# Optimization experiments

Hardware: AMD Instinct MI355X
Metric: run time of the kernel (lower is better)

## Reference

```python
import jax, jax.numpy as jnp
import numpy as np

B, S, D, H = 4, 1024, 1024, 16
HD = D // H  # head_dim = 64
MASKED_BIAS = -10000.0


def setup_inputs() -> dict:
    key = jax.random.key(0)
    ks = jax.random.split(key, 7)
    sc = 0.02
    return {
        "hidden_states": jax.random.normal(ks[0], (B, S, D), jnp.float32),
        "textual_key": jax.random.normal(ks[1], (B, H, S, HD), jnp.float32),
        "textual_value": jax.random.normal(ks[2], (B, H, S, HD), jnp.float32),
        "Wc": jax.random.normal(ks[3], (D, 3 * D), jnp.float32) * sc,  # Conv1D c_attn
        "bc": jnp.zeros((3 * D,), jnp.float32),
        "Wp": jax.random.normal(ks[4], (D, D), jnp.float32) * sc,  # Conv1D c_proj
        "bp": jnp.zeros((D,), jnp.float32),
    }


def reference(hidden_states, textual_key, textual_value, Wc, bc, Wp, bp):
    b, s, d = hidden_states.shape
    # Conv1D: x @ W + b, then split into q, k, v
    qkv = hidden_states @ Wc + bc  # [B,S,3D]
    q, k, v = jnp.split(qkv, 3, axis=-1)

    def split_heads(t):  # [B,S,D] -> [B,H,S,HD]
        return t.reshape(b, s, H, HD).transpose(0, 2, 1, 3)

    q, k, v = split_heads(q), split_heads(k), split_heads(v)

    # cross-key scores against textual past + fused elementwise self-term
    text_w = jnp.einsum("bhqd,bhkd->bhqk", q, textual_key)  # [B,H,S,S_kv]
    self_w = jnp.sum(q * k, axis=-1, keepdims=True)  # [B,H,S,1]
    attn_w = jnp.concatenate([text_w, self_w], axis=-1) / (HD ** 0.5)

    # nonResidual causal mask: bias[kl-ql:kl, 1:kl+1] (strict lower-tri since
    # columns are shifted by 1) concatenated with an always-true self column
    i = jnp.arange(s)
    causal = i[None, :] < i[:, None]  # [S,S_kv]: allow k < q (strict)
    mask = jnp.concatenate([causal, jnp.ones((s, 1), bool)], axis=-1)[None, None]
    attn_w = jnp.where(mask, attn_w, jnp.asarray(MASKED_BIAS, attn_w.dtype))
    attn_w = jax.nn.softmax(attn_w, axis=-1)

    w_rest, w_self = attn_w[..., :-1], attn_w[..., -1:]
    out = jnp.einsum("bhqk,bhkd->bhqd", w_rest, textual_value) + w_self * v

    out = out.transpose(0, 2, 1, 3).reshape(b, s, d)  # merge heads
    return out @ Wp + bp
```

## Files before the change

kernel.cpp:

```cpp
#include <hip/hip_runtime.h>

typedef __bf16 bf16_t;
typedef __bf16 bf16x8 __attribute__((ext_vector_type(8)));
typedef __bf16 bf16x4 __attribute__((ext_vector_type(4)));
typedef float f32x4 __attribute__((ext_vector_type(4)));

__device__ __forceinline__ void gl_lds16(const bf16_t* g, bf16_t* l) {
  __builtin_amdgcn_global_load_lds(
      (const __attribute__((address_space(1))) unsigned int*)g,
      (__attribute__((address_space(3))) unsigned int*)l, 16, 0, 0);
}

__global__ __launch_bounds__(256) void prep_kernel(
    const float* __restrict__ hs, const float* __restrict__ tk, const float* __restrict__ tv,
    const float* __restrict__ Wc, const float* __restrict__ Wp,
    bf16_t* __restrict__ Ahs, bf16_t* __restrict__ Ktb, bf16_t* __restrict__ Vtb,
    bf16_t* __restrict__ WcT, bf16_t* __restrict__ WpT) {
  const int blk = blockIdx.x;
  if (blk < 8192) {
    const float4* src = (blk < 4096) ? (const float4*)hs : (const float4*)tk;
    bf16x4* dst = (blk < 4096) ? (bf16x4*)Ahs : (bf16x4*)Ktb;
    int i = (blk & 4095) * 256 + threadIdx.x;
    float4 v = src[i];
    bf16x4 o;
    o[0] = (bf16_t)v.x; o[1] = (bf16_t)v.y; o[2] = (bf16_t)v.z; o[3] = (bf16_t)v.w;
    dst[i] = o;
  } else {
    __shared__ float tile[32][33];
    const int x = threadIdx.x & 31, y0 = threadIdx.x >> 5;
    const float* in; bf16_t* out; int R, C, c0, r0; size_t base;
    if (blk < 11264) {
      int t = blk - 8192; in = Wc; out = WcT; R = 1024; C = 3072; base = 0;
      c0 = (t % 96) * 32; r0 = (t / 96) * 32;
    } else if (blk < 12288) {
      int t = blk - 11264; in = Wp; out = WpT; R = 1024; C = 1024; base = 0;
      c0 = (t & 31) * 32; r0 = (t >> 5) * 32;
    } else {
      int t = blk - 12288; int z = t >> 6, rest = t & 63;
      in = tv; out = Vtb; R = 1024; C = 64; base = (size_t)z * 65536;
      c0 = (rest & 1) * 32; r0 = (rest >> 1) * 32;
    }
#pragma unroll
    for (int k = 0; k < 4; k++) {
      int y = y0 + 8 * k;
      tile[y][x] = in[base + (size_t)(r0 + y) * C + c0 + x];
    }
    __syncthreads();
#pragma unroll
    for (int k = 0; k < 4; k++) {
      int y = y0 + 8 * k;
      out[base + (size_t)(c0 + y) * R + r0 + x] = (bf16_t)tile[x][y];
    }
  }
}

__global__ __launch_bounds__(256) void gemm_qkv_kernel(
    const bf16_t* __restrict__ A, const bf16_t* __restrict__ Bt, const float* __restrict__ bias,
    bf16_t* __restrict__ Qo, bf16_t* __restrict__ Ko, bf16_t* __restrict__ Vo) {
  __shared__ __align__(16) bf16_t smem[16384];
  bf16_t* Asm = smem;
  bf16_t* Bsm = smem + 8192;
  const int tid = threadIdx.x;
  const int wave = tid >> 6, lane = tid & 63;
  const int c = lane & 15, qd = lane >> 4;
  const int wm = (wave & 1) * 64, wn = (wave >> 1) * 64;
  const int m0 = blockIdx.y * 128, n0 = blockIdx.x * 128;

  f32x4 acc[4][4];
#pragma unroll
  for (int i = 0; i < 4; i++)
#pragma unroll
    for (int j = 0; j < 4; j++) acc[i][j] = (f32x4){0.f, 0.f, 0.f, 0.f};

  for (int kt = 0; kt < 1024; kt += 64) {
#pragma unroll
    for (int p = 0; p < 4; p++) {
      int chunk = p * 256 + tid;
      int row = chunk >> 3, sb = chunk & 7;
      int kb = sb ^ (row & 7);
      gl_lds16(A + (size_t)(m0 + row) * 1024 + kt + kb * 8, &Asm[chunk * 8]);
      gl_lds16(Bt + (size_t)(n0 + row) * 1024 + kt + kb * 8, &Bsm[chunk * 8]);
    }
    __syncthreads();
#pragma unroll
    for (int kk = 0; kk < 2; kk++) {
      bf16x8 af[4], bfr[4];
#pragma unroll
      for (int i = 0; i < 4; i++) {
        int row = wm + 16 * i + c;
        af[i] = *(const bf16x8*)(&Asm[row * 64 + (((4 * kk + qd) ^ (row & 7)) << 3)]);
      }
#pragma unroll
      for (int j = 0; j < 4; j++) {
        int row = wn + 16 * j + c;
        bfr[j] = *(const bf16x8*)(&Bsm[row * 64 + (((4 * kk + qd) ^ (row & 7)) << 3)]);
      }
#pragma unroll
      for (int i = 0; i < 4; i++)
#pragma unroll
        for (int j = 0; j < 4; j++)
          acc[i][j] = __builtin_amdgcn_mfma_f32_16x16x32_bf16(af[i], bfr[j], acc[i][j], 0, 0, 0);
    }
    __syncthreads();
  }
#pragma unroll
  for (int j = 0; j < 4; j++) {
    int n = n0 + wn + 16 * j + c;
    float bv = bias[n];
    int col = wn + 16 * j + c;
#pragma unroll
    for (int i = 0; i < 4; i++) {
#pragma unroll
      for (int r = 0; r < 4; r++) {
        int row = wm + 16 * i + 4 * qd + r;
        int chunk = col >> 3;
        smem[row * 128 + (((chunk ^ (row & 15)) << 3)) + (col & 7)] = (bf16_t)(acc[i][j][r] + bv);
      }
    }
  }
  __syncthreads();
  {
    int row = tid >> 1, half = tid & 1;
    int m = m0 + row, bb = m >> 10, s = m & 1023;
    int nb = n0 + half * 64;
    int type = nb >> 10, d = nb & 1023, h = d >> 6;
    bf16_t* dst = ((type == 0) ? Qo : (type == 1) ? Ko : Vo) +
                  (((size_t)bb * 16 + h) * 1024 + s) * 64;
#pragma unroll
    for (int k = 0; k < 8; k++) {
      int chunk = half * 8 + k;
      bf16x8 v = *(const bf16x8*)(&smem[row * 128 + ((chunk ^ (row & 15)) << 3)]);
      *(bf16x8*)(dst + k * 8) = v;
    }
  }
}

__global__ __launch_bounds__(256) void gemm_out_kernel(
    const bf16_t* __restrict__ A, const bf16_t* __restrict__ Bt, const float* __restrict__ bias,
    float* __restrict__ out) {
  __shared__ bf16_t Asm[2][8192];
  __shared__ bf16_t Bsm[2][8192];
  const int tid = threadIdx.x;
  const int wave = tid >> 6, lane = tid & 63;
  const int c = lane & 15, qd = lane >> 4;
  const int wm = (wave & 1) * 64, wn = (wave >> 1) * 64;
  const int m0 = blockIdx.y * 128, n0 = blockIdx.x * 128;

  f32x4 acc[4][4];
#pragma unroll
  for (int i = 0; i < 4; i++)
#pragma unroll
    for (int j = 0; j < 4; j++) acc[i][j] = (f32x4){0.f, 0.f, 0.f, 0.f};

#pragma unroll
  for (int p = 0; p < 4; p++) {
    int chunk = p * 256 + tid;
    int row = chunk >> 3, sb = chunk & 7;
    int kb = sb ^ (row & 7);
    gl_lds16(A + (size_t)(m0 + row) * 1024 + kb * 8, &Asm[0][chunk * 8]);
    gl_lds16(Bt + (size_t)(n0 + row) * 1024 + kb * 8, &Bsm[0][chunk * 8]);
  }
  for (int it = 0; it < 16; it++) {
    __syncthreads();
    if (it < 15) {
      int nbuf = (it + 1) & 1, kt = (it + 1) * 64;
#pragma unroll
      for (int p = 0; p < 4; p++) {
        int chunk = p * 256 + tid;
        int row = chunk >> 3, sb = chunk & 7;
        int kb = sb ^ (row & 7);
        gl_lds16(A + (size_t)(m0 + row) * 1024 + kt + kb * 8, &Asm[nbuf][chunk * 8]);
        gl_lds16(Bt + (size_t)(n0 + row) * 1024 + kt + kb * 8, &Bsm[nbuf][chunk * 8]);
      }
    }
    const int bs = it & 1;
#pragma unroll
    for (int kk = 0; kk < 2; kk++) {
      bf16x8 af[4], bfr[4];
#pragma unroll
      for (int i = 0; i < 4; i++) {
        int row = wm + 16 * i + c;
        af[i] = *(const bf16x8*)(&Asm[bs][row * 64 + (((4 * kk + qd) ^ (row & 7)) << 3)]);
      }
#pragma unroll
      for (int j = 0; j < 4; j++) {
        int row = wn + 16 * j + c;
        bfr[j] = *(const bf16x8*)(&Bsm[bs][row * 64 + (((4 * kk + qd) ^ (row & 7)) << 3)]);
      }
#pragma unroll
      for (int i = 0; i < 4; i++)
#pragma unroll
        for (int j = 0; j < 4; j++)
          acc[i][j] = __builtin_amdgcn_mfma_f32_16x16x32_bf16(af[i], bfr[j], acc[i][j], 0, 0, 0);
    }
  }
#pragma unroll
  for (int j = 0; j < 4; j++) {
    int n = n0 + wn + 16 * j + c;
    float bv = bias[n];
#pragma unroll
    for (int i = 0; i < 4; i++) {
#pragma unroll
      for (int r = 0; r < 4; r++) {
        int m = m0 + wm + 16 * i + 4 * qd + r;
        out[(size_t)m * 1024 + n] = acc[i][j][r] + bv;
      }
    }
  }
}

#define ATTN_M 12.0f
__global__ __launch_bounds__(512) void attn_kernel(
    const bf16_t* __restrict__ Q, const bf16_t* __restrict__ K, const bf16_t* __restrict__ V,
    const bf16_t* __restrict__ Ktxt, const bf16_t* __restrict__ VtxtT,
    bf16_t* __restrict__ Aout) {
  const int raw = blockIdx.x;
  const int h = blockIdx.y, b = blockIdx.z;
  const int qt = ((b >> 1) & 1) ? (7 - raw) : raw;
  const int bh = b * 16 + h;
  const int tid = threadIdx.x, wave = tid >> 6, lane = tid & 63;
  const int c = lane & 15, qd = lane >> 4;
  const int i_base = qt * 128 + wave * 16;
  const int kt_max = 2 * qt + 1;

  const bf16_t* Qb = Q + (size_t)bh * 65536;
  const bf16_t* Kb = K + (size_t)bh * 65536;
  const bf16_t* Vb = V + (size_t)bh * 65536;
  const bf16_t* Ktb = Ktxt + (size_t)bh * 65536;
  const bf16_t* Vtb = VtxtT + (size_t)bh * 65536;

  __shared__ bf16_t Ksm[2][4096];
  __shared__ bf16_t Vsm[2][4096];
  __shared__ bf16_t Psm[8][1024];

  {
    int row = tid >> 3, sb = tid & 7, kb = sb ^ (row & 7);
    gl_lds16(Ktb + (size_t)row * 64 + kb * 8, &Ksm[0][tid * 8]);
    gl_lds16(Vtb + (size_t)row * 1024 + kb * 8, &Vsm[0][tid * 8]);
  }

  bf16x8 aq[2], kf0, kf1;
  {
    const size_t ro = (size_t)(i_base + c) * 64;
    aq[0] = *(const bf16x8*)(Qb + ro + 8 * qd);
    aq[1] = *(const bf16x8*)(Qb + ro + 32 + 8 * qd);
    kf0 = *(const bf16x8*)(Kb + ro + 8 * qd);
    kf1 = *(const bf16x8*)(Kb + ro + 32 + 8 * qd);
  }
  float part = 0.f;
#pragma unroll
  for (int jj = 0; jj < 8; jj++)
    part += (float)aq[0][jj] * (float)kf0[jj] + (float)aq[1][jj] * (float)kf1[jj];
  part += __shfl_xor(part, 16, 64);
  part += __shfl_xor(part, 32, 64);

  float wself[4], l_part[4];
  f32x4 O[4];
#pragma unroll
  for (int r = 0; r < 4; r++) {
    wself[r] = __expf(__shfl(part, 4 * qd + r, 64) * 0.125f - ATTN_M);
    l_part[r] = 0.f;
  }
#pragma unroll
  for (int t = 0; t < 4; t++)
#pragma unroll
    for (int r = 0; r < 4; r++)
      O[t][r] = wself[r] * (float)Vb[(size_t)(i_base + 4 * qd + r) * 64 + 16 * t + c];

  for (int kt = 0; kt <= kt_max; kt++) {
    __syncthreads();
    if (kt < kt_max) {
      int nb = (kt + 1) & 1;
      int row = tid >> 3, sb = tid & 7, kb = sb ^ (row & 7);
      gl_lds16(Ktb + (size_t)((kt + 1) * 64 + row) * 64 + kb * 8, &Ksm[nb][tid * 8]);
      gl_lds16(Vtb + (size_t)row * 1024 + (kt + 1) * 64 + kb * 8, &Vsm[nb][tid * 8]);
    }
    if (64 * kt >= i_base + 16) continue;
    const int bs = kt & 1;

    f32x4 sc[4];
#pragma unroll
    for (int t = 0; t < 4; t++) sc[t] = (f32x4){0.f, 0.f, 0.f, 0.f};
#pragma unroll
    for (int kk = 0; kk < 2; kk++) {
#pragma unroll
      for (int t = 0; t < 4; t++) {
        int row = 16 * t + c;
        bf16x8 bk = *(const bf16x8*)(&Ksm[bs][row * 64 + (((4 * kk + qd) ^ (row & 7)) << 3)]);
        sc[t] = __builtin_amdgcn_mfma_f32_16x16x32_bf16(aq[kk], bk, sc[t], 0, 0, 0);
      }
    }
    const bool edge = (64 * kt + 63 >= i_base);
    if (!edge) {
#pragma unroll
      for (int t = 0; t < 4; t++)
#pragma unroll
        for (int r = 0; r < 4; r++) {
          float p = __expf(sc[t][r] * 0.125f - ATTN_M);
          l_part[r] += p;
          sc[t][r] = p;
        }
    } else {
#pragma unroll
      for (int t = 0; t < 4; t++)
#pragma unroll
        for (int r = 0; r < 4; r++) {
          bool masked = (64 * kt + 16 * t + c >= i_base + 4 * qd + r);
          float p = masked ? 0.f : __expf(sc[t][r] * 0.125f - ATTN_M);
          l_part[r] += p;
          sc[t][r] = p;
        }
    }
#pragma unroll
    for (int t = 0; t < 4; t++) {
#pragma unroll
      for (int r = 0; r < 4; r++) {
        int row = 4 * qd + r;
        int col = 16 * t + c;
        Psm[wave][row * 64 + (((col >> 3) ^ (row & 7)) << 3) + (col & 7)] = (bf16_t)sc[t][r];
      }
    }
#pragma unroll
    for (int kk = 0; kk < 2; kk++) {
      bf16x8 ap = *(const bf16x8*)(&Psm[wave][c * 64 + (((4 * kk + qd) ^ (c & 7)) << 3)]);
#pragma unroll
      for (int u = 0; u < 4; u++) {
        int row = 16 * u + c;
        bf16x8 bv = *(const bf16x8*)(&Vsm[bs][row * 64 + (((4 * kk + qd) ^ (row & 7)) << 3)]);
        O[u] = __builtin_amdgcn_mfma_f32_16x16x32_bf16(ap, bv, O[u], 0, 0, 0);
      }
    }
  }

#pragma unroll
  for (int r = 0; r < 4; r++) {
#pragma unroll
    for (int mk = 1; mk < 16; mk <<= 1) l_part[r] += __shfl_xor(l_part[r], mk, 64);
    float inv = 1.0f / (l_part[r] + wself[r]);
    int i = i_base + 4 * qd + r;
#pragma unroll
    for (int u = 0; u < 4; u++)
      Aout[((size_t)b * 1024 + i) * 1024 + h * 64 + 16 * u + c] = (bf16_t)(O[u][r] * inv);
  }
}

extern "C" void kernel_launch(void* const* d_in, const int* in_sizes, int n_in,
                              void* d_out, int out_size, void* d_ws, size_t ws_size,
                              hipStream_t stream) {
  const float* hs = (const float*)d_in[0];
  const float* tk = (const float*)d_in[1];
  const float* tv = (const float*)d_in[2];
  const float* Wc = (const float*)d_in[3];
  const float* bc = (const float*)d_in[4];
  const float* Wp = (const float*)d_in[5];
  const float* bp = (const float*)d_in[6];
  float* out = (float*)d_out;

  bf16_t* ws = (bf16_t*)d_ws;
  const size_t M1 = 1u << 20;
  bf16_t* Ahs  = ws;
  bf16_t* WcT  = ws + 4 * M1;
  bf16_t* WpT  = ws + 7 * M1;
  bf16_t* Ktb  = ws + 8 * M1;
  bf16_t* Vtb  = ws + 12 * M1;
  bf16_t* Qb   = ws + 16 * M1;
  bf16_t* Kb   = ws + 20 * M1;
  bf16_t* Vb   = ws + 24 * M1;
  bf16_t* Aout = ws + 28 * M1;

  prep_kernel<<<16384, 256, 0, stream>>>(hs, tk, tv, Wc, Wp, Ahs, Ktb, Vtb, WcT, WpT);
  gemm_qkv_kernel<<<dim3(24, 32), 256, 0, stream>>>(Ahs, WcT, bc, Qb, Kb, Vb);
  attn_kernel<<<dim3(8, 16, 4), 512, 0, stream>>>(Qb, Kb, Vb, Ktb, Vtb, Aout);
  gemm_out_kernel<<<dim3(8, 32), 256, 0, stream>>>(Aout, WpT, bp, out);
}
```

Measured before the change: 207.8 us.

## Remap QKV GEMM blocks per XCD, drop LDS-staged epilogue, reorder attention grid

The QKV GEMM now remaps its linear block id so that each XCD handles a contiguous group of N tiles, which should improve L2 reuse of the weight matrix. Its epilogue drops the LDS transpose staging and its vectorized stores, and instead writes scalar bf16 values straight to the head-split Q/K/V layout. The attention grid is reordered so that all 64 batch-heads of one q-tile launch together. This removes the old per-batch reversal of q-tile order used to balance load. The scalar 2-byte stores may be less coalesced, and launching the causal tiles in order may leave the GPU unevenly loaded at the tail.

Result: faster. 203.4 us (-2.1%).

```diff
diff --git a/kernel.cpp b/kernel.cpp
--- a/kernel.cpp
+++ b/kernel.cpp
@@ -57,14 +57,15 @@
 __global__ __launch_bounds__(256) void gemm_qkv_kernel(
     const bf16_t* __restrict__ A, const bf16_t* __restrict__ Bt, const float* __restrict__ bias,
     bf16_t* __restrict__ Qo, bf16_t* __restrict__ Ko, bf16_t* __restrict__ Vo) {
-  __shared__ __align__(16) bf16_t smem[16384];
-  bf16_t* Asm = smem;
-  bf16_t* Bsm = smem + 8192;
+  __shared__ __align__(16) bf16_t Asm[128 * 64];
+  __shared__ __align__(16) bf16_t Bsm[128 * 64];
   const int tid = threadIdx.x;
   const int wave = tid >> 6, lane = tid & 63;
   const int c = lane & 15, qd = lane >> 4;
   const int wm = (wave & 1) * 64, wn = (wave >> 1) * 64;
-  const int m0 = blockIdx.y * 128, n0 = blockIdx.x * 128;
+  const int id = blockIdx.y * 24 + blockIdx.x;
+  const int xcd = id & 7, idx = id >> 3;
+  const int n0 = (xcd * 3 + (idx % 3)) * 128, m0 = (idx / 3) * 128;
 
   f32x4 acc[4][4];
 #pragma unroll
@@ -107,30 +108,17 @@
   for (int j = 0; j < 4; j++) {
     int n = n0 + wn + 16 * j + c;
     float bv = bias[n];
-    int col = wn + 16 * j + c;
+    int type = n >> 10, d = n & 1023;
+    int h = d >> 6, hd = d & 63;
+    bf16_t* dst = (type == 0) ? Qo : (type == 1) ? Ko : Vo;
 #pragma unroll
     for (int i = 0; i < 4; i++) {
 #pragma unroll
       for (int r = 0; r < 4; r++) {
-        int row = wm + 16 * i + 4 * qd + r;
-        int chunk = col >> 3;
-        smem[row * 128 + (((chunk ^ (row & 15)) << 3)) + (col & 7)] = (bf16_t)(acc[i][j][r] + bv);
-      }
-    }
-  }
-  __syncthreads();
-  {
-    int row = tid >> 1, half = tid & 1;
-    int m = m0 + row, bb = m >> 10, s = m & 1023;
-    int nb = n0 + half * 64;
-    int type = nb >> 10, d = nb & 1023, h = d >> 6;
-    bf16_t* dst = ((type == 0) ? Qo : (type == 1) ? Ko : Vo) +
-                  (((size_t)bb * 16 + h) * 1024 + s) * 64;
-#pragma unroll
-    for (int k = 0; k < 8; k++) {
-      int chunk = half * 8 + k;
-      bf16x8 v = *(const bf16x8*)(&smem[row * 128 + ((chunk ^ (row & 15)) << 3)]);
-      *(bf16x8*)(dst + k * 8) = v;
+        int m = m0 + wm + 16 * i + 4 * qd + r;
+        int bb = m >> 10, s = m & 1023;
+        dst[(((size_t)bb * 16 + h) * 1024 + s) * 64 + hd] = (bf16_t)(acc[i][j][r] + bv);
+      }
     }
   }
 }
@@ -214,10 +202,9 @@
     const bf16_t* __restrict__ Q, const bf16_t* __restrict__ K, const bf16_t* __restrict__ V,
     const bf16_t* __restrict__ Ktxt, const bf16_t* __restrict__ VtxtT,
     bf16_t* __restrict__ Aout) {
-  const int raw = blockIdx.x;
-  const int h = blockIdx.y, b = blockIdx.z;
-  const int qt = ((b >> 1) & 1) ? (7 - raw) : raw;
-  const int bh = b * 16 + h;
+  const int bh = blockIdx.x;
+  const int qt = blockIdx.y;
+  const int b = bh >> 4, h = bh & 15;
   const int tid = threadIdx.x, wave = tid >> 6, lane = tid & 63;
   const int c = lane & 15, qd = lane >> 4;
   const int i_base = qt * 128 + wave * 16;
@@ -370,6 +357,6 @@
 
   prep_kernel<<<16384, 256, 0, stream>>>(hs, tk, tv, Wc, Wp, Ahs, Ktb, Vtb, WcT, WpT);
   gemm_qkv_kernel<<<dim3(24, 32), 256, 0, stream>>>(Ahs, WcT, bc, Qb, Kb, Vb);
-  attn_kernel<<<dim3(8, 16, 4), 512, 0, stream>>>(Qb, Kb, Vb, Ktb, Vtb, Aout);
+  attn_kernel<<<dim3(64, 8), 512, 0, stream>>>(Qb, Kb, Vb, Ktb, Vtb, Aout);
   gemm_out_kernel<<<dim3(8, 32), 256, 0, stream>>>(Aout, WpT, bp, out);
 }
```
